# Performance work log

Measured on AMD Instinct MI355X. Metric: run time of the kernel, lower is better.

## Reference

```python
import jax, jax.numpy as jnp
import numpy as np

N_NODES = 100000
N_EDGES = 1600000
IN_FEATS = 256
OUT_FEATS = 128


def setup_inputs() -> dict:
    key = jax.random.key(0)
    k1, k2, k3, k4 = jax.random.split(key, 4)
    feat = jax.random.normal(k1, (N_NODES, IN_FEATS), dtype=jnp.float32)
    src = jax.random.randint(k2, (N_EDGES,), 0, N_NODES, dtype=jnp.int64)
    dst = jax.random.randint(k3, (N_EDGES,), 0, N_NODES, dtype=jnp.int64)
    W = jax.random.normal(k4, (IN_FEATS, OUT_FEATS), dtype=jnp.float32) * (1.0 / np.sqrt(IN_FEATS))
    b = jnp.zeros((OUT_FEATS,), dtype=jnp.float32)
    return {"feat": feat, "src": src, "dst": dst, "W": W, "b": b}


def reference(feat, src, dst, W, b):
    # norm = 'both': symmetric degree normalization, clip degrees at 1
    ones = jnp.ones((src.shape[0],), dtype=jnp.float32)
    out_deg = jax.ops.segment_sum(ones, src, num_segments=N_NODES)  # out-degree per src node
    in_deg = jax.ops.segment_sum(ones, dst, num_segments=N_NODES)   # in-degree per dst node
    norm_src = jnp.power(jnp.clip(out_deg, 1.0, None), -0.5)[:, None]  # (N,1)
    norm_dst = jnp.power(jnp.clip(in_deg, 1.0, None), -0.5)[:, None]   # (N,1)

    h = feat * norm_src
    # in_feats (256) > out_feats (128): apply W before aggregation
    h = h @ W  # (N, out_feats)
    # copy_src + sum aggregation over edges (SpMM)
    msgs = h[src]  # (E, out_feats)
    rst = jax.ops.segment_sum(msgs, dst, num_segments=N_NODES)  # (N, out_feats)
    rst = rst * norm_dst
    rst = rst + b
    return rst
```

## Files before the change

### kernel.cpp

```cpp
#include <hip/hip_runtime.h>
#include <hip/hip_bf16.h>
#include <cstddef>

#define NN 100000
#define NE 1600000
#define INF 256
#define OUTF 128
#define NBKT 196
#define BSH 9
#define P1B 250
#define EPB 6400
#define SCL (NBKT * P1B)
#define SCLP 49152

typedef __bf16 bf16x8 __attribute__((ext_vector_type(8)));
typedef float f32x4 __attribute__((ext_vector_type(4)));

__device__ __forceinline__ float bflo(uint v) { return __uint_as_float(v << 16); }
__device__ __forceinline__ float bfhi(uint v) { return __uint_as_float(v & 0xffff0000u); }

__global__ __launch_bounds__(256) void k_p1a(const int* __restrict__ src,
                                             const int* __restrict__ dst,
                                             int* __restrict__ ghd,
                                             int* __restrict__ ghs,
                                             const float* __restrict__ W,
                                             __bf16* __restrict__ Wt) {
  if (blockIdx.x >= P1B) {
    int i = (blockIdx.x - P1B) * 256 + threadIdx.x;
    if (i < SCLP - SCL) { ghd[SCL + i] = 0; ghs[SCL + i] = 0; }
    int n = i & 127, k = i >> 7;
    Wt[n * INF + k] = (__bf16)W[k * OUTF + n];
    return;
  }
  __shared__ int lhd[NBKT], lhs[NBKT];
  const int t = threadIdx.x;
  if (t < NBKT) { lhd[t] = 0; lhs[t] = 0; }
  __syncthreads();
  const int base = blockIdx.x * EPB;
#pragma unroll
  for (int i = 0; i < EPB / 256; ++i) {
    int e = base + i * 256 + t;
    atomicAdd(&lhd[dst[e] >> BSH], 1);
    atomicAdd(&lhs[src[e] >> BSH], 1);
  }
  __syncthreads();
  if (t < NBKT) {
    ghd[t * P1B + blockIdx.x] = lhd[t];
    ghs[t * P1B + blockIdx.x] = lhs[t];
  }
}

__global__ __launch_bounds__(1024) void k_p1b(int* __restrict__ ghd,
                                              int* __restrict__ ghs,
                                              int* __restrict__ row_start) {
  int* a = blockIdx.x ? ghs : ghd;
  __shared__ int wsum[16];
  const int t = threadIdx.x;
  const int lane = t & 63, wid = t >> 6;
  int4 v[12];
  const int4* p = (const int4*)(a + t * 48);
#pragma unroll
  for (int i = 0; i < 12; ++i) v[i] = p[i];
  int s = 0;
#pragma unroll
  for (int i = 0; i < 12; ++i) s += v[i].x + v[i].y + v[i].z + v[i].w;
  const int mysum = s;
#pragma unroll
  for (int d = 1; d < 64; d <<= 1) {
    int u = __shfl_up(s, d);
    if (lane >= d) s += u;
  }
  if (lane == 63) wsum[wid] = s;
  __syncthreads();
  if (wid == 0) {
    int ws = (lane < 16) ? wsum[lane] : 0;
    int inc = ws;
#pragma unroll
    for (int d = 1; d < 16; d <<= 1) {
      int u = __shfl_up(inc, d);
      if (lane >= d) inc += u;
    }
    if (lane < 16) wsum[lane] = inc - ws;
  }
  __syncthreads();
  int ex = wsum[wid] + s - mysum;
#pragma unroll
  for (int i = 0; i < 12; ++i) {
    int4 w;
    w.x = ex; ex += v[i].x;
    w.y = ex; ex += v[i].y;
    w.z = ex; ex += v[i].z;
    w.w = ex; ex += v[i].w;
    ((int4*)(a + t * 48))[i] = w;
  }
  if (blockIdx.x == 0 && t == 0) row_start[NN] = NE;
}

__global__ __launch_bounds__(256) void k_p1c(const int* __restrict__ src,
                                             const int* __restrict__ dst,
                                             const int* __restrict__ ghd,
                                             const int* __restrict__ ghs,
                                             uint* __restrict__ rec_d,
                                             ushort* __restrict__ rec_s) {
  __shared__ int od[NBKT], os[NBKT];
  const int t = threadIdx.x;
  if (t < NBKT) {
    od[t] = ghd[t * P1B + blockIdx.x];
    os[t] = ghs[t * P1B + blockIdx.x];
  }
  __syncthreads();
  const int base = blockIdx.x * EPB;
#pragma unroll
  for (int i = 0; i < EPB / 256; ++i) {
    int e = base + i * 256 + t;
    int s = src[e], d = dst[e];
    int p = atomicAdd(&od[d >> BSH], 1);
    rec_d[p] = ((uint)s << BSH) | (uint)(d & 511);
    int q = atomicAdd(&os[s >> BSH], 1);
    rec_s[q] = (ushort)(s & 511);
  }
}

__global__ __launch_bounds__(256) void k_p2(const int* __restrict__ ghd,
                                            const int* __restrict__ ghs,
                                            const uint* __restrict__ rec_d,
                                            const ushort* __restrict__ rec_s,
                                            int* __restrict__ edge_src,
                                            int* __restrict__ row_start,
                                            float* __restrict__ ns) {
  __shared__ int lh[512];
  __shared__ int sc[256];
  const int k = blockIdx.x, t = threadIdx.x;
  {
    const int base = ghd[k * P1B];
    const int end = (k == NBKT - 1) ? NE : ghd[(k + 1) * P1B];
    lh[t] = 0; lh[t + 256] = 0;
    __syncthreads();
    for (int j = base + t; j < end; j += 256) atomicAdd(&lh[rec_d[j] & 511], 1);
    __syncthreads();
    int a0 = lh[2 * t], a1 = lh[2 * t + 1];
    sc[t] = a0 + a1;
    __syncthreads();
    for (int off = 1; off < 256; off <<= 1) {
      int add = (t >= off) ? sc[t - off] : 0;
      __syncthreads();
      sc[t] += add;
      __syncthreads();
    }
    int ex = t ? sc[t - 1] : 0;
    int e0 = ex, e1 = ex + a0;
    int n0 = k * 512 + 2 * t;
    if (n0 < NN) row_start[n0] = base + e0;
    if (n0 + 1 < NN) row_start[n0 + 1] = base + e1;
    __syncthreads();
    lh[2 * t] = base + e0;
    lh[2 * t + 1] = base + e1;
    __syncthreads();
    for (int j = base + t; j < end; j += 256) {
      uint r = rec_d[j];
      int p = atomicAdd(&lh[r & 511], 1);
      edge_src[p] = (int)(r >> BSH);
    }
  }
  __syncthreads();
  {
    const int base = ghs[k * P1B];
    const int end = (k == NBKT - 1) ? NE : ghs[(k + 1) * P1B];
    lh[t] = 0; lh[t + 256] = 0;
    __syncthreads();
    for (int j = base + t; j < end; j += 256) atomicAdd(&lh[rec_s[j]], 1);
    __syncthreads();
    int n0 = k * 512 + t, n1 = n0 + 256;
    if (n0 < NN) { int c = lh[t];       ns[n0] = rsqrtf((float)(c > 1 ? c : 1)); }
    if (n1 < NN) { int c = lh[t + 256]; ns[n1] = rsqrtf((float)(c > 1 ? c : 1)); }
  }
}

__global__ __launch_bounds__(256) void k_gemm(const float* __restrict__ feat,
                                              const __bf16* __restrict__ Wt,
                                              __bf16* __restrict__ h) {
  const int w = threadIdx.x >> 6, l = threadIdx.x & 63;
  const int lr = l & 15, lg = l >> 4;
  const int row0 = blockIdx.x * 64 + (w >> 1) * 32;
  const int col0 = (w & 1) * 64;

  bf16x8 bf[4][8];
  const __bf16* bp = Wt + (size_t)(col0 + lr) * INF + lg * 8;
#pragma unroll
  for (int nf = 0; nf < 4; ++nf)
#pragma unroll
    for (int kk = 0; kk < 8; ++kk)
      bf[nf][kk] = *(const bf16x8*)(bp + (size_t)nf * 16 * INF + kk * 32);

  f32x4 acc[2][4];
#pragma unroll
  for (int i = 0; i < 2; ++i)
#pragma unroll
    for (int j = 0; j < 4; ++j) acc[i][j] = (f32x4)0.0f;

  int r0 = row0 + lr;      if (r0 >= NN) r0 = NN - 1;
  int r1 = row0 + 16 + lr; if (r1 >= NN) r1 = NN - 1;
  const float* ap0 = feat + (size_t)r0 * INF + lg * 8;
  const float* ap1 = feat + (size_t)r1 * INF + lg * 8;

  float4 c0l = *(const float4*)(ap0);
  float4 c0h = *(const float4*)(ap0 + 4);
  float4 c1l = *(const float4*)(ap1);
  float4 c1h = *(const float4*)(ap1 + 4);

#pragma unroll
  for (int kk = 0; kk < 8; ++kk) {
    float4 n0l, n0h, n1l, n1h;
    if (kk < 7) {
      const float* p0 = ap0 + (kk + 1) * 32;
      const float* p1 = ap1 + (kk + 1) * 32;
      n0l = *(const float4*)(p0);
      n0h = *(const float4*)(p0 + 4);
      n1l = *(const float4*)(p1);
      n1h = *(const float4*)(p1 + 4);
    }
    bf16x8 a0, a1;
    a0[0] = (__bf16)c0l.x; a0[1] = (__bf16)c0l.y; a0[2] = (__bf16)c0l.z; a0[3] = (__bf16)c0l.w;
    a0[4] = (__bf16)c0h.x; a0[5] = (__bf16)c0h.y; a0[6] = (__bf16)c0h.z; a0[7] = (__bf16)c0h.w;
    a1[0] = (__bf16)c1l.x; a1[1] = (__bf16)c1l.y; a1[2] = (__bf16)c1l.z; a1[3] = (__bf16)c1l.w;
    a1[4] = (__bf16)c1h.x; a1[5] = (__bf16)c1h.y; a1[6] = (__bf16)c1h.z; a1[7] = (__bf16)c1h.w;
#pragma unroll
    for (int nf = 0; nf < 4; ++nf) {
      acc[0][nf] = __builtin_amdgcn_mfma_f32_16x16x32_bf16(a0, bf[nf][kk], acc[0][nf], 0, 0, 0);
      acc[1][nf] = __builtin_amdgcn_mfma_f32_16x16x32_bf16(a1, bf[nf][kk], acc[1][nf], 0, 0, 0);
    }
    c0l = n0l; c0h = n0h; c1l = n1l; c1h = n1h;
  }

#pragma unroll
  for (int mf = 0; mf < 2; ++mf) {
#pragma unroll
    for (int r = 0; r < 4; ++r) {
      int row = row0 + mf * 16 + lg * 4 + r;
      if (row < NN) {
        __bf16* hp = h + (size_t)row * OUTF + col0 + lr;
#pragma unroll
        for (int nf = 0; nf < 4; ++nf)
          hp[nf * 16] = (__bf16)(acc[mf][nf][r]);
      }
    }
  }
}

__global__ __launch_bounds__(256) void k_aggr(const uint4* __restrict__ h4,
                                              const int* __restrict__ row_start,
                                              const float* __restrict__ ns,
                                              const int* __restrict__ edge_src,
                                              const float* __restrict__ bias,
                                              float* __restrict__ out) {
  const int wave = threadIdx.x >> 6;
  const int lane = threadIdx.x & 63;
  const int q = lane >> 4;
  const int cl = lane & 15;
  const int n = blockIdx.x * 4 + wave;
  const int s0 = row_start[n];
  const int s1 = row_start[n + 1];
  const int cnt = s1 - s0;

  float a0 = 0.f, a1 = 0.f, a2 = 0.f, a3 = 0.f, a4 = 0.f, a5 = 0.f, a6 = 0.f, a7 = 0.f;
  for (int j0 = 0; j0 < cnt; j0 += 64) {
    int nb = cnt - j0; if (nb > 64) nb = 64;
    int idv = 0; float nsv = 0.f;
    if (lane < nb) idv = edge_src[s0 + j0 + lane];
    if (lane < nb) nsv = ns[idv];
#pragma unroll 4
    for (int j = 0; j < nb; j += 4) {
      int jj = j + q;
      int e = __shfl(idv, jj);
      float w = __shfl(nsv, jj);
      if (jj < nb) {
        uint4 v = h4[(size_t)e * 16 + cl];
        a0 += w * bflo(v.x); a1 += w * bfhi(v.x);
        a2 += w * bflo(v.y); a3 += w * bfhi(v.y);
        a4 += w * bflo(v.z); a5 += w * bfhi(v.z);
        a6 += w * bflo(v.w); a7 += w * bfhi(v.w);
      }
    }
  }
  a0 += __shfl_xor(a0, 16); a1 += __shfl_xor(a1, 16); a2 += __shfl_xor(a2, 16); a3 += __shfl_xor(a3, 16);
  a4 += __shfl_xor(a4, 16); a5 += __shfl_xor(a5, 16); a6 += __shfl_xor(a6, 16); a7 += __shfl_xor(a7, 16);
  a0 += __shfl_xor(a0, 32); a1 += __shfl_xor(a1, 32); a2 += __shfl_xor(a2, 32); a3 += __shfl_xor(a3, 32);
  a4 += __shfl_xor(a4, 32); a5 += __shfl_xor(a5, 32); a6 += __shfl_xor(a6, 32); a7 += __shfl_xor(a7, 32);

  if (q == 0) {
    float ndv = rsqrtf((float)(cnt > 1 ? cnt : 1));
    const float4* b4 = (const float4*)bias;
    float4 ba = b4[2 * cl], bb = b4[2 * cl + 1];
    float4 o0, o1;
    o0.x = a0 * ndv + ba.x; o0.y = a1 * ndv + ba.y; o0.z = a2 * ndv + ba.z; o0.w = a3 * ndv + ba.w;
    o1.x = a4 * ndv + bb.x; o1.y = a5 * ndv + bb.y; o1.z = a6 * ndv + bb.z; o1.w = a7 * ndv + bb.w;
    float4* op = (float4*)(out + (size_t)n * OUTF);
    op[2 * cl] = o0;
    op[2 * cl + 1] = o1;
  }
}

extern "C" void kernel_launch(void* const* d_in, const int* in_sizes, int n_in,
                              void* d_out, int out_size, void* d_ws, size_t ws_size,
                              hipStream_t stream) {
  const float* feat = (const float*)d_in[0];
  const int* src = (const int*)d_in[1];
  const int* dst = (const int*)d_in[2];
  const float* Wm = (const float*)d_in[3];
  const float* bias = (const float*)d_in[4];
  float* out = (float*)d_out;

  char* ws = (char*)d_ws;
  __bf16* h        = (__bf16*)(ws + 0);
  __bf16* Wt       = (__bf16*)(ws + 25600000);
  int*    ghd      = (int*)(ws + 25665536);
  int*    ghs      = (int*)(ws + 25862144);
  uint*   rec_d    = (uint*)(ws + 26058752);
  ushort* rec_s    = (ushort*)(ws + 32458752);
  int*    edge_src = (int*)(ws + 35658752);
  int*    row_start= (int*)(ws + 42058752);
  float*  ns       = (float*)(ws + 42458768);

  k_p1a<<<P1B + 128, 256, 0, stream>>>(src, dst, ghd, ghs, Wm, Wt);
  k_p1b<<<2, 1024, 0, stream>>>(ghd, ghs, row_start);
  k_p1c<<<P1B, 256, 0, stream>>>(src, dst, ghd, ghs, rec_d, rec_s);
  k_p2<<<NBKT, 256, 0, stream>>>(ghd, ghs, rec_d, rec_s, edge_src, row_start, ns);
  k_gemm<<<(NN + 63) / 64, 256, 0, stream>>>(feat, Wt, h);
  k_aggr<<<NN / 4, 256, 0, stream>>>((const uint4*)h, row_start, ns, edge_src, bias, out);
}
```

Measured before the change: 196.9 us.

## Stage feat tiles through LDS with async global_load_lds double buffering in GEMM

The GEMM kernel now loads 128-row by 64-column fp32 feat tiles into a double-buffered, XOR-swizzled LDS buffer using global_load_lds. The next K-tile load overlaps the MFMA work on the current one. Each wave now computes all 128 output columns for 32 rows and reloads W fragments per K-tile from global memory, instead of holding the whole W slice in registers. This is meant to hide feat load latency and cut register pressure, at the cost of 64KB of LDS per block, block-wide barriers, and repeated W fetches.

```diff
diff --git a/kernel.cpp b/kernel.cpp
--- a/kernel.cpp
+++ b/kernel.cpp
@@ -18,6 +18,11 @@
 
 __device__ __forceinline__ float bflo(uint v) { return __uint_as_float(v << 16); }
 __device__ __forceinline__ float bfhi(uint v) { return __uint_as_float(v & 0xffff0000u); }
+
+__device__ __forceinline__ void gload16(const void* g, void* l) {
+  __builtin_amdgcn_global_load_lds((const __attribute__((address_space(1))) void*)g,
+                                   (__attribute__((address_space(3))) void*)l, 16, 0, 0);
+}
 
 __global__ __launch_bounds__(256) void k_p1a(const int* __restrict__ src,
                                              const int* __restrict__ dst,
@@ -176,75 +181,84 @@
   }
 }
 
-__global__ __launch_bounds__(256) void k_gemm(const float* __restrict__ feat,
-                                              const __bf16* __restrict__ Wt,
-                                              __bf16* __restrict__ h) {
-  const int w = threadIdx.x >> 6, l = threadIdx.x & 63;
+__global__ __launch_bounds__(256, 2) void k_gemm(const float* __restrict__ feat,
+                                                 const __bf16* __restrict__ Wt,
+                                                 __bf16* __restrict__ h) {
+  __shared__ float lA[2][128 * 64];
+  const int tid = threadIdx.x;
+  const int w = tid >> 6, l = tid & 63;
   const int lr = l & 15, lg = l >> 4;
-  const int row0 = blockIdx.x * 64 + (w >> 1) * 32;
-  const int col0 = (w & 1) * 64;
-
-  bf16x8 bf[4][8];
-  const __bf16* bp = Wt + (size_t)(col0 + lr) * INF + lg * 8;
-#pragma unroll
-  for (int nf = 0; nf < 4; ++nf)
-#pragma unroll
-    for (int kk = 0; kk < 8; ++kk)
-      bf[nf][kk] = *(const bf16x8*)(bp + (size_t)nf * 16 * INF + kk * 32);
-
-  f32x4 acc[2][4];
+  const int bm = blockIdx.x * 128;
+
+#define STAGE(b, t)                                                            \
+  {                                                                            \
+    _Pragma("unroll")                                                          \
+    for (int i = 0; i < 8; ++i) {                                              \
+      int chunk = i * 256 + tid;                                               \
+      int row = chunk >> 4, cp = chunk & 15;                                   \
+      int gr = bm + row; if (gr >= NN) gr = NN - 1;                            \
+      int sc = cp ^ (row & 7);                                                 \
+      gload16(feat + (size_t)gr * INF + (t) * 64 + sc * 4,                     \
+              &lA[b][0] + (size_t)chunk * 4);                                  \
+    }                                                                          \
+  }
+
+  STAGE(0, 0);
+
+  f32x4 acc[2][8];
 #pragma unroll
   for (int i = 0; i < 2; ++i)
 #pragma unroll
-    for (int j = 0; j < 4; ++j) acc[i][j] = (f32x4)0.0f;
-
-  int r0 = row0 + lr;      if (r0 >= NN) r0 = NN - 1;
-  int r1 = row0 + 16 + lr; if (r1 >= NN) r1 = NN - 1;
-  const float* ap0 = feat + (size_t)r0 * INF + lg * 8;
-  const float* ap1 = feat + (size_t)r1 * INF + lg * 8;
-
-  float4 c0l = *(const float4*)(ap0);
-  float4 c0h = *(const float4*)(ap0 + 4);
-  float4 c1l = *(const float4*)(ap1);
-  float4 c1h = *(const float4*)(ap1 + 4);
-
-#pragma unroll
-  for (int kk = 0; kk < 8; ++kk) {
-    float4 n0l, n0h, n1l, n1h;
-    if (kk < 7) {
-      const float* p0 = ap0 + (kk + 1) * 32;
-      const float* p1 = ap1 + (kk + 1) * 32;
-      n0l = *(const float4*)(p0);
-      n0h = *(const float4*)(p0 + 4);
-      n1l = *(const float4*)(p1);
-      n1h = *(const float4*)(p1 + 4);
-    }
-    bf16x8 a0, a1;
-    a0[0] = (__bf16)c0l.x; a0[1] = (__bf16)c0l.y; a0[2] = (__bf16)c0l.z; a0[3] = (__bf16)c0l.w;
-    a0[4] = (__bf16)c0h.x; a0[5] = (__bf16)c0h.y; a0[6] = (__bf16)c0h.z; a0[7] = (__bf16)c0h.w;
-    a1[0] = (__bf16)c1l.x; a1[1] = (__bf16)c1l.y; a1[2] = (__bf16)c1l.z; a1[3] = (__bf16)c1l.w;
-    a1[4] = (__bf16)c1h.x; a1[5] = (__bf16)c1h.y; a1[6] = (__bf16)c1h.z; a1[7] = (__bf16)c1h.w;
-#pragma unroll
-    for (int nf = 0; nf < 4; ++nf) {
-      acc[0][nf] = __builtin_amdgcn_mfma_f32_16x16x32_bf16(a0, bf[nf][kk], acc[0][nf], 0, 0, 0);
-      acc[1][nf] = __builtin_amdgcn_mfma_f32_16x16x32_bf16(a1, bf[nf][kk], acc[1][nf], 0, 0, 0);
-    }
-    c0l = n0l; c0h = n0h; c1l = n1l; c1h = n1h;
+    for (int j = 0; j < 8; ++j) acc[i][j] = (f32x4)0.0f;
+
+  __syncthreads();
+
+  for (int t = 0; t < 4; ++t) {
+    if (t < 3) STAGE((t + 1) & 1, t + 1);
+    const float* lb = &lA[t & 1][0];
+    const __bf16* bp = Wt + (size_t)lr * INF + t * 64 + lg * 8;
+    bf16x8 bfrag[2][8];
+#pragma unroll
+    for (int kk = 0; kk < 2; ++kk)
+#pragma unroll
+      for (int nf = 0; nf < 8; ++nf)
+        bfrag[kk][nf] = *(const bf16x8*)(bp + (size_t)nf * 16 * INF + kk * 32);
+#pragma unroll
+    for (int kk = 0; kk < 2; ++kk) {
+#pragma unroll
+      for (int mf = 0; mf < 2; ++mf) {
+        int row = w * 32 + mf * 16 + lr;
+        int c = kk * 8 + lg * 2;
+        f32x4 x0 = *(const f32x4*)(lb + row * 64 + ((c ^ (row & 7)) << 2));
+        f32x4 x1 = *(const f32x4*)(lb + row * 64 + (((c + 1) ^ (row & 7)) << 2));
+        bf16x8 a;
+#pragma unroll
+        for (int j = 0; j < 4; ++j) {
+          a[j] = (__bf16)x0[j];
+          a[4 + j] = (__bf16)x1[j];
+        }
+#pragma unroll
+        for (int nf = 0; nf < 8; ++nf)
+          acc[mf][nf] = __builtin_amdgcn_mfma_f32_16x16x32_bf16(a, bfrag[kk][nf], acc[mf][nf], 0, 0, 0);
+      }
+    }
+    __syncthreads();
   }
 
 #pragma unroll
   for (int mf = 0; mf < 2; ++mf) {
 #pragma unroll
     for (int r = 0; r < 4; ++r) {
-      int row = row0 + mf * 16 + lg * 4 + r;
+      int row = bm + w * 32 + mf * 16 + lg * 4 + r;
       if (row < NN) {
-        __bf16* hp = h + (size_t)row * OUTF + col0 + lr;
-#pragma unroll
-        for (int nf = 0; nf < 4; ++nf)
+        __bf16* hp = h + (size_t)row * OUTF + lr;
+#pragma unroll
+        for (int nf = 0; nf < 8; ++nf)
           hp[nf * 16] = (__bf16)(acc[mf][nf][r]);
       }
     }
   }
+#undef STAGE
 }
 
 __global__ __launch_bounds__(256) void k_aggr(const uint4* __restrict__ h4,
@@ -325,6 +339,6 @@
   k_p1b<<<2, 1024, 0, stream>>>(ghd, ghs, row_start);
   k_p1c<<<P1B, 256, 0, stream>>>(src, dst, ghd, ghs, rec_d, rec_s);
   k_p2<<<NBKT, 256, 0, stream>>>(ghd, ghs, rec_d, rec_s, edge_src, row_start, ns);
-  k_gemm<<<(NN + 63) / 64, 256, 0, stream>>>(feat, Wt, h);
+  k_gemm<<<(NN + 127) / 128, 256, 0, stream>>>(feat, Wt, h);
   k_aggr<<<NN / 4, 256, 0, stream>>>((const uint4*)h, row_start, ns, edge_src, bias, out);
 }
```

Measured after the change: 186.2 us. 1.06x faster.
